# Performance work log

Measured on AMD Instinct MI355X. Metric: run time of the kernel, lower is better.

The kernel has to match this reference:

```python
import jax, jax.numpy as jnp
from jax import lax
import numpy as np

DN = ('NCHW', 'OIHW', 'NCHW')

def conv2d(x, w, b, stride=1, padding=1):
    out = lax.conv_general_dilated(
        x, w, window_strides=(stride, stride),
        padding=[(padding, padding), (padding, padding)],
        dimension_numbers=DN)
    return out + b[None, :, None, None]

def maxpool2d(x, k=2, s=2):
    return lax.reduce_window(x, -jnp.inf, lax.max,
                             window_dimensions=(1, 1, k, k),
                             window_strides=(1, 1, s, s),
                             padding='VALID')

def setup_inputs() -> dict:
    key = jax.random.key(0)
    ks = jax.random.split(key, 9)
    B = 4096
    x = jax.random.normal(ks[0], (B, 3, 32, 32), dtype=jnp.float32)
    # weights initialized like torch.randn(...) * 0.1, biases zeros
    w1 = jax.random.normal(ks[1], (16, 3, 3, 3), dtype=jnp.float32) * 0.1
    b1 = jnp.zeros((16,), jnp.float32)
    w2 = jax.random.normal(ks[2], (32, 16, 3, 3), dtype=jnp.float32) * 0.1
    b2 = jnp.zeros((32,), jnp.float32)
    w3 = jax.random.normal(ks[3], (64, 32, 3, 3), dtype=jnp.float32) * 0.1
    b3 = jnp.zeros((64,), jnp.float32)
    # fc: Linear(64*4*4, 10); kaiming-uniform-ish init
    fan_in = 64 * 4 * 4
    bound = 1.0 / np.sqrt(fan_in)
    fc_w = jax.random.uniform(ks[4], (10, fan_in), jnp.float32, -bound, bound)
    fc_b = jax.random.uniform(ks[5], (10,), jnp.float32, -bound, bound)
    return {"x": x, "w1": w1, "b1": b1, "w2": w2, "b2": b2,
            "w3": w3, "b3": b3, "fc_w": fc_w, "fc_b": fc_b}

def reference(x, w1, b1, w2, b2, w3, b3, fc_w, fc_b):
    h = maxpool2d(jax.nn.relu(conv2d(x, w1, b1)))   # [B,16,16,16]
    h = maxpool2d(jax.nn.relu(conv2d(h, w2, b2)))   # [B,32,8,8]
    h = maxpool2d(jax.nn.relu(conv2d(h, w3, b3)))   # [B,64,4,4]
    h = h.reshape(h.shape[0], -1)                    # [B,1024]
    # dropout is identity in eval mode
    return h @ fc_w.T + fc_b
```

## Files before the change

kernel.cpp:

```cpp
#include <hip/hip_runtime.h>

typedef float f32x4 __attribute__((ext_vector_type(4)));
typedef float f32x16v __attribute__((ext_vector_type(16)));
typedef __bf16 bf16x4 __attribute__((ext_vector_type(4)));
typedef __bf16 bf16x8 __attribute__((ext_vector_type(8)));

union U4B8 { uint4 u; bf16x8 b; };

#define B2P_OFF 0
#define B3P_OFF 9216
#define C1P_OFF 46080

__global__ __launch_bounds__(256) void pack_weights(
    const float* __restrict__ w1, const float* __restrict__ w2,
    const float* __restrict__ w3, __bf16* __restrict__ wsb) {
  int i = blockIdx.x * 256 + threadIdx.x;
  if (i < 9216) {
    int f = i >> 9, r = i & 511;
    int l = r >> 3, j = r & 7;
    int t = f >> 1, p = f & 1;
    int ky = t / 3, kx = t % 3;
    int oc = l & 31, ic = ((l >> 5) << 3) + j;
    float v = w2[oc * 144 + ic * 9 + ky * 3 + kx];
    __bf16 hi = (__bf16)v;
    wsb[B2P_OFF + i] = p ? (__bf16)(v - (float)hi) : hi;
  } else if (i < 9216 + 36864) {
    int q = i - 9216;
    int f = q >> 9, r = q & 511;
    int l = r >> 3, j = r & 7;
    int t = f >> 3, nt = (f >> 1) & 3, p = f & 1;
    int ky = t / 3, kx = t % 3;
    int oc = nt * 16 + (l & 15), ic = ((l >> 4) << 3) + j;
    float v = w3[oc * 288 + ic * 9 + ky * 3 + kx];
    __bf16 hi = (__bf16)v;
    wsb[B3P_OFF + q] = p ? (__bf16)(v - (float)hi) : hi;
  } else if (i < 9216 + 36864 + 1024) {
    int q = i - (9216 + 36864);
    int f = q >> 9, r = q & 511;
    int l = r >> 3, j = r & 7;
    int oc = l & 15, k = ((l >> 4) << 3) + j;
    float v = 0.f;
    if (k < 27) {
      int kx = k / 9, rem = k % 9;
      int ky = rem / 3, ic = rem % 3;
      v = w1[oc * 27 + ic * 9 + ky * 3 + kx];
    }
    __bf16 hi = (__bf16)v;
    wsb[C1P_OFF + q] = f ? (__bf16)(v - (float)hi) : hi;
  }
}

__global__ __launch_bounds__(256, 4) void cnn_fused(
    const float* __restrict__ x, const __bf16* __restrict__ wsb,
    const float* __restrict__ b1, const float* __restrict__ b2,
    const float* __restrict__ b3,
    const float* __restrict__ fcw, const float* __restrict__ fcb,
    float* __restrict__ out) {
  __shared__ __align__(16) unsigned char smem[16128];
  __bf16* s_img = (__bf16*)smem;
  __bf16* s2b   = (__bf16*)smem;
  __bf16* s3b   = (__bf16*)smem;
  float*  h3s   = (float*)(smem + 8960);

  const __bf16* b2p = wsb + B2P_OFF;
  const __bf16* b3p = wsb + B3P_OFF;
  const __bf16* c1p = wsb + C1P_OFF;

  const int tid = threadIdx.x;
  const int img = blockIdx.x;
  const int w = tid >> 6, lane = tid & 63;

  if (tid < 132) {
    int row, col;
    if (tid < 34)       { row = 0;        col = tid; }
    else if (tid < 68)  { row = 33;       col = tid - 34; }
    else if (tid < 100) { row = tid - 67; col = 0; }
    else                { row = tid - 99; col = 33; }
    *(unsigned long long*)&s_img[(row * 34 + col) * 4] = 0ull;
  }
  const float* xg = x + img * 3072;
  for (int i = tid; i < 1024; i += 256) {
    const int y = i >> 5, xx = i & 31;
    bf16x4 pk;
    pk.x = (__bf16)xg[i];
    pk.y = (__bf16)xg[i + 1024];
    pk.z = (__bf16)xg[i + 2048];
    pk.w = (__bf16)0.f;
    *(bf16x4*)&s_img[((y + 1) * 34 + (xx + 1)) * 4] = pk;
  }
  const bf16x8 B1h = *(const bf16x8*)(c1p + lane * 8);
  const bf16x8 B1l = *(const bf16x8*)(c1p + 512 + lane * 8);
  __syncthreads();

  float pooled[16];
  {
    const int xm = lane & 15, kg = lane >> 4;
    #pragma unroll
    for (int p = 0; p < 4; ++p) {
      f32x4 acc[2][2];
      #pragma unroll
      for (int ys = 0; ys < 2; ++ys)
        #pragma unroll
        for (int xh = 0; xh < 2; ++xh)
          #pragma unroll
          for (int r = 0; r < 4; ++r) acc[ys][xh][r] = 0.f;
      #pragma unroll
      for (int ys = 0; ys < 2; ++ys) {
        const int yqg = w * 8 + p * 2 + ys;
        #pragma unroll
        for (int xh = 0; xh < 2; ++xh) {
          const int xv = xh * 16 + xm;
          const int ca = xv + (kg <= 1 ? 0 : kg - 1);
          const int cb = xv + (kg < 2 ? 1 : 2);
          const uint2 qa0 = *(const uint2*)&s_img[((yqg + 0) * 34 + ca) * 4];
          const uint2 qa1 = *(const uint2*)&s_img[((yqg + 1) * 34 + ca) * 4];
          const uint2 qa2 = *(const uint2*)&s_img[((yqg + 2) * 34 + ca) * 4];
          const uint2 qb0 = *(const uint2*)&s_img[((yqg + 0) * 34 + cb) * 4];
          const uint2 qb1 = *(const uint2*)&s_img[((yqg + 1) * 34 + cb) * 4];
          const uint2 qb2 = *(const uint2*)&s_img[((yqg + 2) * 34 + cb) * 4];
          const uint a0 = qa0.x, a1 = qa0.y, a2 = qa1.x, a3 = qa1.y, a4 = qa2.x, a5 = qa2.y;
          const uint b0 = qb0.x, b1 = qb0.y, b2 = qb1.x, b3 = qb1.y, b4 = qb2.x;
          U4B8 A;
          A.u.x = kg == 0 ? a0
                : kg == 1 ? (a5 | (b0 << 16))
                : kg == 2 ? ((a4 >> 16) | (a5 << 16))
                :           a4;
          A.u.y = kg == 0 ? (a1 | (a2 << 16))
                : kg == 1 ? ((b0 >> 16) | (b1 << 16))
                : kg == 2 ? b0
                :           a5;
          A.u.z = kg == 0 ? ((a2 >> 16) | (a3 << 16))
                : kg == 1 ? b2
                : kg == 2 ? (b1 | (b2 << 16))
                :           0u;
          A.u.w = kg == 0 ? a4
                : kg == 1 ? (b3 | (b4 << 16))
                : kg == 2 ? ((b2 >> 16) | (b3 << 16))
                :           0u;
          acc[ys][xh] = __builtin_amdgcn_mfma_f32_16x16x32_bf16(A.b, B1h, acc[ys][xh], 0, 0, 0);
          acc[ys][xh] = __builtin_amdgcn_mfma_f32_16x16x32_bf16(A.b, B1l, acc[ys][xh], 0, 0, 0);
        }
      }
      #pragma unroll
      for (int xh = 0; xh < 2; ++xh)
        #pragma unroll
        for (int xp2 = 0; xp2 < 2; ++xp2) {
          const float v0 = fmaxf(acc[0][xh][xp2 * 2], acc[0][xh][xp2 * 2 + 1]);
          const float v1 = fmaxf(acc[1][xh][xp2 * 2], acc[1][xh][xp2 * 2 + 1]);
          pooled[p * 4 + xh * 2 + xp2] = fmaxf(v0, v1);
        }
    }
  }
  __syncthreads();

  if (tid < 68) {
    int row, col;
    if (tid < 18)      { row = 0;       col = tid; }
    else if (tid < 36) { row = 17;      col = tid - 18; }
    else if (tid < 52) { row = tid - 35; col = 0; }
    else               { row = tid - 51; col = 17; }
    unsigned long long* p = (unsigned long long*)&s2b[row * 448 + col * 24];
    p[0] = 0ull; p[1] = 0ull; p[2] = 0ull; p[3] = 0ull;
  }
  {
    const int oc = lane & 15, quad = lane >> 4;
    const float bias = b1[oc];
    #pragma unroll
    for (int p = 0; p < 4; ++p)
      #pragma unroll
      for (int xh = 0; xh < 2; ++xh)
        #pragma unroll
        for (int xp2 = 0; xp2 < 2; ++xp2) {
          const float v = fmaxf(pooled[p * 4 + xh * 2 + xp2] + bias, 0.f);
          const int py = w * 4 + p, px = xh * 8 + quad * 2 + xp2;
          s2b[(py + 1) * 448 + (px + 1) * 24 + oc] = (__bf16)v;
        }
  }
  bf16x8 Bf[18];
  #pragma unroll
  for (int f = 0; f < 18; ++f)
    Bf[f] = *(const bf16x8*)(b2p + f * 512 + lane * 8);
  __syncthreads();

  float pooled2[8];
  {
    const unsigned short* s2 = (const unsigned short*)s2b;
    const int xm = lane & 15, yoff = (lane >> 4) & 1, kh = lane >> 5;
    f32x16v acc0, acc1;
    #pragma unroll
    for (int r = 0; r < 16; ++r) { acc0[r] = 0.f; acc1[r] = 0.f; }
    #pragma unroll
    for (int t = 0; t < 9; ++t) {
      const int ky = t / 3, kx = t % 3;
      const int col = (xm + kx) * 24 + kh * 8;
      const int row0 = (4 * w + yoff + ky) * 448 + col;
      const int row1 = row0 + 896;
      bf16x8 a0h = *(const bf16x8*)&s2[row0];
      bf16x8 a1h = *(const bf16x8*)&s2[row1];
      acc0 = __builtin_amdgcn_mfma_f32_32x32x16_bf16(a0h, Bf[t * 2],     acc0, 0, 0, 0);
      acc1 = __builtin_amdgcn_mfma_f32_32x32x16_bf16(a1h, Bf[t * 2],     acc1, 0, 0, 0);
      acc0 = __builtin_amdgcn_mfma_f32_32x32x16_bf16(a0h, Bf[t * 2 + 1], acc0, 0, 0, 0);
      acc1 = __builtin_amdgcn_mfma_f32_32x32x16_bf16(a1h, Bf[t * 2 + 1], acc1, 0, 0, 0);
    }
    #pragma unroll
    for (int i2 = 0; i2 < 2; ++i2) {
      const f32x16v& a = i2 ? acc1 : acc0;
      #pragma unroll
      for (int bq = 0; bq < 2; ++bq)
        #pragma unroll
        for (int rq = 0; rq < 2; ++rq) {
          const int r0 = bq * 4 + rq * 2;
          pooled2[i2 * 4 + bq * 2 + rq] =
              fmaxf(fmaxf(a[r0], a[r0 + 1]), fmaxf(a[r0 + 8], a[r0 + 9]));
        }
    }
  }
  __syncthreads();

  if (tid < 36) {
    int row, col;
    if (tid < 10)      { row = 0;       col = tid; }
    else if (tid < 20) { row = 9;       col = tid - 10; }
    else if (tid < 28) { row = tid - 19; col = 0; }
    else               { row = tid - 27; col = 9; }
    unsigned long long* p = (unsigned long long*)&s3b[row * 448 + col * 40];
    #pragma unroll
    for (int u = 0; u < 8; ++u) p[u] = 0ull;
  }
  {
    const int oc = lane & 31, hh = lane >> 5;
    const float bias = b2[oc];
    #pragma unroll
    for (int i2 = 0; i2 < 2; ++i2)
      #pragma unroll
      for (int bq = 0; bq < 2; ++bq)
        #pragma unroll
        for (int rq = 0; rq < 2; ++rq) {
          const float v = fmaxf(pooled2[i2 * 4 + bq * 2 + rq] + bias, 0.f);
          const int py = 2 * w + i2, px = 2 * hh + 4 * bq + rq;
          s3b[(py + 1) * 448 + (px + 1) * 40 + oc] = (__bf16)v;
        }
  }
  __syncthreads();

  {
    const unsigned short* s3 = (const unsigned short*)s3b;
    const int nt = w;
    bf16x8 Bt[18];
    #pragma unroll
    for (int t = 0; t < 9; ++t) {
      Bt[t * 2]     = *(const bf16x8*)(b3p + (t * 8 + nt * 2) * 512 + lane * 8);
      Bt[t * 2 + 1] = *(const bf16x8*)(b3p + (t * 8 + nt * 2 + 1) * 512 + lane * 8);
    }
    const int m = lane & 15, quad = lane >> 4;
    const int xm = m & 7, yoff = m >> 3;
    f32x4 acc[4];
    #pragma unroll
    for (int mt = 0; mt < 4; ++mt)
      #pragma unroll
      for (int r = 0; r < 4; ++r) acc[mt][r] = 0.f;
    #pragma unroll
    for (int t = 0; t < 9; ++t) {
      const int ky = t / 3, kx = t % 3;
      #pragma unroll
      for (int mt = 0; mt < 4; ++mt) {
        const int ro = (2 * mt + yoff + ky) * 448 + (xm + kx) * 40 + quad * 8;
        bf16x8 ah = *(const bf16x8*)&s3[ro];
        acc[mt] = __builtin_amdgcn_mfma_f32_16x16x32_bf16(ah, Bt[t * 2],     acc[mt], 0, 0, 0);
        acc[mt] = __builtin_amdgcn_mfma_f32_16x16x32_bf16(ah, Bt[t * 2 + 1], acc[mt], 0, 0, 0);
      }
    }
    const int ocl = lane & 15;
    #pragma unroll
    for (int mt = 0; mt < 4; ++mt) {
      float p0 = fmaxf(acc[mt][0], acc[mt][1]);
      float p1 = fmaxf(acc[mt][2], acc[mt][3]);
      p0 = fmaxf(p0, __shfl_xor(p0, 32, 64));
      p1 = fmaxf(p1, __shfl_xor(p1, 32, 64));
      if (quad < 2) {
        const int oc = nt * 16 + ocl;
        const float bias = b3[oc];
        const int base = oc * 16 + mt * 4 + (quad & 1) * 2;
        h3s[base]     = fmaxf(p0 + bias, 0.f);
        h3s[base + 1] = fmaxf(p1 + bias, 0.f);
      }
    }
  }
  __syncthreads();

  if (w == 0) {
    float hv[16];
    #pragma unroll
    for (int i = 0; i < 16; ++i) hv[i] = h3s[i * 64 + lane];
    #pragma unroll
    for (int j = 0; j < 10; ++j) {
      float dot = 0.f;
      #pragma unroll
      for (int i = 0; i < 16; ++i)
        dot = fmaf(hv[i], fcw[j * 1024 + i * 64 + lane], dot);
      #pragma unroll
      for (int s = 32; s > 0; s >>= 1) dot += __shfl_xor(dot, s, 64);
      if (lane == 0) out[img * 10 + j] = dot + fcb[j];
    }
  }
}

extern "C" void kernel_launch(void* const* d_in, const int* in_sizes, int n_in,
                              void* d_out, int out_size, void* d_ws, size_t ws_size,
                              hipStream_t stream) {
  const float* x   = (const float*)d_in[0];
  const float* w1  = (const float*)d_in[1];
  const float* b1  = (const float*)d_in[2];
  const float* w2  = (const float*)d_in[3];
  const float* b2  = (const float*)d_in[4];
  const float* w3  = (const float*)d_in[5];
  const float* b3  = (const float*)d_in[6];
  const float* fcw = (const float*)d_in[7];
  const float* fcb = (const float*)d_in[8];
  __bf16* wsb = (__bf16*)d_ws;
  float* out = (float*)d_out;

  hipLaunchKernelGGL(pack_weights, dim3(184), dim3(256), 0, stream, w1, w2, w3, wsb);
  hipLaunchKernelGGL(cnn_fused, dim3(4096), dim3(256), 0, stream,
                     x, wsb, b1, b2, b3, fcw, fcb, out);
}
```

Baseline: 155.8 us.

## Process two images per block to amortize weight register loads

Each block now handles two images instead of one, halving the grid to 2048 blocks and doubling shared memory to about 32KB. The per-wave weight fragments for conv2 and conv3 are loaded into registers once and reused across both images, and the loop over images sits inside each stage, so barriers are shared as well. The FC stage uses two waves, one per image. The cost is more shared memory per block and more register pressure from the doubled pooled arrays, which could reduce occupancy, along with fewer blocks overall.

```diff
diff --git a/kernel.cpp b/kernel.cpp
--- a/kernel.cpp
+++ b/kernel.cpp
@@ -56,125 +56,134 @@
     const float* __restrict__ b3,
     const float* __restrict__ fcw, const float* __restrict__ fcb,
     float* __restrict__ out) {
-  __shared__ __align__(16) unsigned char smem[16128];
+  __shared__ __align__(16) unsigned char smem[32256];
   __bf16* s_img = (__bf16*)smem;
   __bf16* s2b   = (__bf16*)smem;
   __bf16* s3b   = (__bf16*)smem;
-  float*  h3s   = (float*)(smem + 8960);
+  float*  h3s   = (float*)(smem + 17920);
 
   const __bf16* b2p = wsb + B2P_OFF;
   const __bf16* b3p = wsb + B3P_OFF;
   const __bf16* c1p = wsb + C1P_OFF;
 
   const int tid = threadIdx.x;
-  const int img = blockIdx.x;
+  const int img0 = blockIdx.x * 2;
   const int w = tid >> 6, lane = tid & 63;
 
-  if (tid < 132) {
+  for (int i = tid; i < 264; i += 256) {
+    int ik = i >= 132, c = ik ? i - 132 : i;
     int row, col;
-    if (tid < 34)       { row = 0;        col = tid; }
-    else if (tid < 68)  { row = 33;       col = tid - 34; }
-    else if (tid < 100) { row = tid - 67; col = 0; }
-    else                { row = tid - 99; col = 33; }
-    *(unsigned long long*)&s_img[(row * 34 + col) * 4] = 0ull;
-  }
-  const float* xg = x + img * 3072;
-  for (int i = tid; i < 1024; i += 256) {
-    const int y = i >> 5, xx = i & 31;
+    if (c < 34)       { row = 0;       col = c; }
+    else if (c < 68)  { row = 33;      col = c - 34; }
+    else if (c < 100) { row = c - 67;  col = 0; }
+    else              { row = c - 99;  col = 33; }
+    *(unsigned long long*)&s_img[ik * 4624 + (row * 34 + col) * 4] = 0ull;
+  }
+  for (int i = tid; i < 2048; i += 256) {
+    const int ik = i >> 10, rem = i & 1023;
+    const int y = rem >> 5, xx = rem & 31;
+    const float* xg = x + (img0 + ik) * 3072;
     bf16x4 pk;
-    pk.x = (__bf16)xg[i];
-    pk.y = (__bf16)xg[i + 1024];
-    pk.z = (__bf16)xg[i + 2048];
+    pk.x = (__bf16)xg[rem];
+    pk.y = (__bf16)xg[rem + 1024];
+    pk.z = (__bf16)xg[rem + 2048];
     pk.w = (__bf16)0.f;
-    *(bf16x4*)&s_img[((y + 1) * 34 + (xx + 1)) * 4] = pk;
+    *(bf16x4*)&s_img[ik * 4624 + ((y + 1) * 34 + (xx + 1)) * 4] = pk;
   }
   const bf16x8 B1h = *(const bf16x8*)(c1p + lane * 8);
   const bf16x8 B1l = *(const bf16x8*)(c1p + 512 + lane * 8);
   __syncthreads();
 
-  float pooled[16];
+  float pooled[2][16];
   {
     const int xm = lane & 15, kg = lane >> 4;
     #pragma unroll
-    for (int p = 0; p < 4; ++p) {
-      f32x4 acc[2][2];
-      #pragma unroll
-      for (int ys = 0; ys < 2; ++ys)
+    for (int ik = 0; ik < 2; ++ik) {
+      const __bf16* si = s_img + ik * 4624;
+      #pragma unroll
+      for (int p = 0; p < 4; ++p) {
+        f32x4 acc[2][2];
+        #pragma unroll
+        for (int ys = 0; ys < 2; ++ys)
+          #pragma unroll
+          for (int xh = 0; xh < 2; ++xh)
+            #pragma unroll
+            for (int r = 0; r < 4; ++r) acc[ys][xh][r] = 0.f;
+        #pragma unroll
+        for (int ys = 0; ys < 2; ++ys) {
+          const int yqg = w * 8 + p * 2 + ys;
+          #pragma unroll
+          for (int xh = 0; xh < 2; ++xh) {
+            const int xv = xh * 16 + xm;
+            const int ca = xv + (kg <= 1 ? 0 : kg - 1);
+            const int cb = xv + (kg < 2 ? 1 : 2);
+            const uint2 qa0 = *(const uint2*)&si[((yqg + 0) * 34 + ca) * 4];
+            const uint2 qa1 = *(const uint2*)&si[((yqg + 1) * 34 + ca) * 4];
+            const uint2 qa2 = *(const uint2*)&si[((yqg + 2) * 34 + ca) * 4];
+            const uint2 qb0 = *(const uint2*)&si[((yqg + 0) * 34 + cb) * 4];
+            const uint2 qb1 = *(const uint2*)&si[((yqg + 1) * 34 + cb) * 4];
+            const uint2 qb2 = *(const uint2*)&si[((yqg + 2) * 34 + cb) * 4];
+            const uint a0 = qa0.x, a1 = qa0.y, a2 = qa1.x, a3 = qa1.y, a4 = qa2.x, a5 = qa2.y;
+            const uint b0 = qb0.x, b1 = qb0.y, b2 = qb1.x, b3 = qb1.y, b4 = qb2.x;
+            U4B8 A;
+            A.u.x = kg == 0 ? a0
+                  : kg == 1 ? (a5 | (b0 << 16))
+                  : kg == 2 ? ((a4 >> 16) | (a5 << 16))
+                  :           a4;
+            A.u.y = kg == 0 ? (a1 | (a2 << 16))
+                  : kg == 1 ? ((b0 >> 16) | (b1 << 16))
+                  : kg == 2 ? b0
+                  :           a5;
+            A.u.z = kg == 0 ? ((a2 >> 16) | (a3 << 16))
+                  : kg == 1 ? b2
+                  : kg == 2 ? (b1 | (b2 << 16))
+                  :           0u;
+            A.u.w = kg == 0 ? a4
+                  : kg == 1 ? (b3 | (b4 << 16))
+                  : kg == 2 ? ((b2 >> 16) | (b3 << 16))
+                  :           0u;
+            acc[ys][xh] = __builtin_amdgcn_mfma_f32_16x16x32_bf16(A.b, B1h, acc[ys][xh], 0, 0, 0);
+            acc[ys][xh] = __builtin_amdgcn_mfma_f32_16x16x32_bf16(A.b, B1l, acc[ys][xh], 0, 0, 0);
+          }
+        }
         #pragma unroll
         for (int xh = 0; xh < 2; ++xh)
           #pragma unroll
-          for (int r = 0; r < 4; ++r) acc[ys][xh][r] = 0.f;
-      #pragma unroll
-      for (int ys = 0; ys < 2; ++ys) {
-        const int yqg = w * 8 + p * 2 + ys;
-        #pragma unroll
-        for (int xh = 0; xh < 2; ++xh) {
-          const int xv = xh * 16 + xm;
-          const int ca = xv + (kg <= 1 ? 0 : kg - 1);
-          const int cb = xv + (kg < 2 ? 1 : 2);
-          const uint2 qa0 = *(const uint2*)&s_img[((yqg + 0) * 34 + ca) * 4];
-          const uint2 qa1 = *(const uint2*)&s_img[((yqg + 1) * 34 + ca) * 4];
-          const uint2 qa2 = *(const uint2*)&s_img[((yqg + 2) * 34 + ca) * 4];
-          const uint2 qb0 = *(const uint2*)&s_img[((yqg + 0) * 34 + cb) * 4];
-          const uint2 qb1 = *(const uint2*)&s_img[((yqg + 1) * 34 + cb) * 4];
-          const uint2 qb2 = *(const uint2*)&s_img[((yqg + 2) * 34 + cb) * 4];
-          const uint a0 = qa0.x, a1 = qa0.y, a2 = qa1.x, a3 = qa1.y, a4 = qa2.x, a5 = qa2.y;
-          const uint b0 = qb0.x, b1 = qb0.y, b2 = qb1.x, b3 = qb1.y, b4 = qb2.x;
-          U4B8 A;
-          A.u.x = kg == 0 ? a0
-                : kg == 1 ? (a5 | (b0 << 16))
-                : kg == 2 ? ((a4 >> 16) | (a5 << 16))
-                :           a4;
-          A.u.y = kg == 0 ? (a1 | (a2 << 16))
-                : kg == 1 ? ((b0 >> 16) | (b1 << 16))
-                : kg == 2 ? b0
-                :           a5;
-          A.u.z = kg == 0 ? ((a2 >> 16) | (a3 << 16))
-                : kg == 1 ? b2
-                : kg == 2 ? (b1 | (b2 << 16))
-                :           0u;
-          A.u.w = kg == 0 ? a4
-                : kg == 1 ? (b3 | (b4 << 16))
-                : kg == 2 ? ((b2 >> 16) | (b3 << 16))
-                :           0u;
-          acc[ys][xh] = __builtin_amdgcn_mfma_f32_16x16x32_bf16(A.b, B1h, acc[ys][xh], 0, 0, 0);
-          acc[ys][xh] = __builtin_amdgcn_mfma_f32_16x16x32_bf16(A.b, B1l, acc[ys][xh], 0, 0, 0);
-        }
-      }
-      #pragma unroll
-      for (int xh = 0; xh < 2; ++xh)
-        #pragma unroll
-        for (int xp2 = 0; xp2 < 2; ++xp2) {
-          const float v0 = fmaxf(acc[0][xh][xp2 * 2], acc[0][xh][xp2 * 2 + 1]);
-          const float v1 = fmaxf(acc[1][xh][xp2 * 2], acc[1][xh][xp2 * 2 + 1]);
-          pooled[p * 4 + xh * 2 + xp2] = fmaxf(v0, v1);
-        }
-    }
-  }
-  __syncthreads();
-
-  if (tid < 68) {
+          for (int xp2 = 0; xp2 < 2; ++xp2) {
+            const float v0 = fmaxf(acc[0][xh][xp2 * 2], acc[0][xh][xp2 * 2 + 1]);
+            const float v1 = fmaxf(acc[1][xh][xp2 * 2], acc[1][xh][xp2 * 2 + 1]);
+            pooled[ik][p * 4 + xh * 2 + xp2] = fmaxf(v0, v1);
+          }
+      }
+    }
+  }
+  __syncthreads();
+
+  if (tid < 136) {
+    int ik = tid >= 68, c = ik ? tid - 68 : tid;
     int row, col;
-    if (tid < 18)      { row = 0;       col = tid; }
-    else if (tid < 36) { row = 17;      col = tid - 18; }
-    else if (tid < 52) { row = tid - 35; col = 0; }
-    else               { row = tid - 51; col = 17; }
-    unsigned long long* p = (unsigned long long*)&s2b[row * 448 + col * 24];
+    if (c < 18)      { row = 0;       col = c; }
+    else if (c < 36) { row = 17;      col = c - 18; }
+    else if (c < 52) { row = c - 35;  col = 0; }
+    else             { row = c - 51;  col = 17; }
+    unsigned long long* p = (unsigned long long*)&s2b[ik * 8064 + row * 448 + col * 24];
     p[0] = 0ull; p[1] = 0ull; p[2] = 0ull; p[3] = 0ull;
   }
   {
     const int oc = lane & 15, quad = lane >> 4;
     const float bias = b1[oc];
     #pragma unroll
-    for (int p = 0; p < 4; ++p)
-      #pragma unroll
-      for (int xh = 0; xh < 2; ++xh)
-        #pragma unroll
-        for (int xp2 = 0; xp2 < 2; ++xp2) {
-          const float v = fmaxf(pooled[p * 4 + xh * 2 + xp2] + bias, 0.f);
-          const int py = w * 4 + p, px = xh * 8 + quad * 2 + xp2;
-          s2b[(py + 1) * 448 + (px + 1) * 24 + oc] = (__bf16)v;
-        }
+    for (int ik = 0; ik < 2; ++ik)
+      #pragma unroll
+      for (int p = 0; p < 4; ++p)
+        #pragma unroll
+        for (int xh = 0; xh < 2; ++xh)
+          #pragma unroll
+          for (int xp2 = 0; xp2 < 2; ++xp2) {
+            const float v = fmaxf(pooled[ik][p * 4 + xh * 2 + xp2] + bias, 0.f);
+            const int py = w * 4 + p, px = xh * 8 + quad * 2 + xp2;
+            s2b[ik * 8064 + (py + 1) * 448 + (px + 1) * 24 + oc] = (__bf16)v;
+          }
   }
   bf16x8 Bf[18];
   #pragma unroll
@@ -182,48 +191,52 @@
     Bf[f] = *(const bf16x8*)(b2p + f * 512 + lane * 8);
   __syncthreads();
 
-  float pooled2[8];
-  {
-    const unsigned short* s2 = (const unsigned short*)s2b;
+  float pooled2[2][8];
+  {
     const int xm = lane & 15, yoff = (lane >> 4) & 1, kh = lane >> 5;
-    f32x16v acc0, acc1;
-    #pragma unroll
-    for (int r = 0; r < 16; ++r) { acc0[r] = 0.f; acc1[r] = 0.f; }
-    #pragma unroll
-    for (int t = 0; t < 9; ++t) {
-      const int ky = t / 3, kx = t % 3;
-      const int col = (xm + kx) * 24 + kh * 8;
-      const int row0 = (4 * w + yoff + ky) * 448 + col;
-      const int row1 = row0 + 896;
-      bf16x8 a0h = *(const bf16x8*)&s2[row0];
-      bf16x8 a1h = *(const bf16x8*)&s2[row1];
-      acc0 = __builtin_amdgcn_mfma_f32_32x32x16_bf16(a0h, Bf[t * 2],     acc0, 0, 0, 0);
-      acc1 = __builtin_amdgcn_mfma_f32_32x32x16_bf16(a1h, Bf[t * 2],     acc1, 0, 0, 0);
-      acc0 = __builtin_amdgcn_mfma_f32_32x32x16_bf16(a0h, Bf[t * 2 + 1], acc0, 0, 0, 0);
-      acc1 = __builtin_amdgcn_mfma_f32_32x32x16_bf16(a1h, Bf[t * 2 + 1], acc1, 0, 0, 0);
-    }
-    #pragma unroll
-    for (int i2 = 0; i2 < 2; ++i2) {
-      const f32x16v& a = i2 ? acc1 : acc0;
-      #pragma unroll
-      for (int bq = 0; bq < 2; ++bq)
-        #pragma unroll
-        for (int rq = 0; rq < 2; ++rq) {
-          const int r0 = bq * 4 + rq * 2;
-          pooled2[i2 * 4 + bq * 2 + rq] =
-              fmaxf(fmaxf(a[r0], a[r0 + 1]), fmaxf(a[r0 + 8], a[r0 + 9]));
-        }
-    }
-  }
-  __syncthreads();
-
-  if (tid < 36) {
+    #pragma unroll
+    for (int ik = 0; ik < 2; ++ik) {
+      const unsigned short* s2 = (const unsigned short*)s2b + ik * 8064;
+      f32x16v acc0, acc1;
+      #pragma unroll
+      for (int r = 0; r < 16; ++r) { acc0[r] = 0.f; acc1[r] = 0.f; }
+      #pragma unroll
+      for (int t = 0; t < 9; ++t) {
+        const int ky = t / 3, kx = t % 3;
+        const int col = (xm + kx) * 24 + kh * 8;
+        const int row0 = (4 * w + yoff + ky) * 448 + col;
+        const int row1 = row0 + 896;
+        bf16x8 a0h = *(const bf16x8*)&s2[row0];
+        bf16x8 a1h = *(const bf16x8*)&s2[row1];
+        acc0 = __builtin_amdgcn_mfma_f32_32x32x16_bf16(a0h, Bf[t * 2],     acc0, 0, 0, 0);
+        acc1 = __builtin_amdgcn_mfma_f32_32x32x16_bf16(a1h, Bf[t * 2],     acc1, 0, 0, 0);
+        acc0 = __builtin_amdgcn_mfma_f32_32x32x16_bf16(a0h, Bf[t * 2 + 1], acc0, 0, 0, 0);
+        acc1 = __builtin_amdgcn_mfma_f32_32x32x16_bf16(a1h, Bf[t * 2 + 1], acc1, 0, 0, 0);
+      }
+      #pragma unroll
+      for (int i2 = 0; i2 < 2; ++i2) {
+        const f32x16v& a = i2 ? acc1 : acc0;
+        #pragma unroll
+        for (int bq = 0; bq < 2; ++bq)
+          #pragma unroll
+          for (int rq = 0; rq < 2; ++rq) {
+            const int r0 = bq * 4 + rq * 2;
+            pooled2[ik][i2 * 4 + bq * 2 + rq] =
+                fmaxf(fmaxf(a[r0], a[r0 + 1]), fmaxf(a[r0 + 8], a[r0 + 9]));
+          }
+      }
+    }
+  }
+  __syncthreads();
+
+  if (tid < 72) {
+    int ik = tid >= 36, c = ik ? tid - 36 : tid;
     int row, col;
-    if (tid < 10)      { row = 0;       col = tid; }
-    else if (tid < 20) { row = 9;       col = tid - 10; }
-    else if (tid < 28) { row = tid - 19; col = 0; }
-    else               { row = tid - 27; col = 9; }
-    unsigned long long* p = (unsigned long long*)&s3b[row * 448 + col * 40];
+    if (c < 10)      { row = 0;       col = c; }
+    else if (c < 20) { row = 9;       col = c - 10; }
+    else if (c < 28) { row = c - 19;  col = 0; }
+    else             { row = c - 27;  col = 9; }
+    unsigned long long* p = (unsigned long long*)&s3b[ik * 4480 + row * 448 + col * 40];
     #pragma unroll
     for (int u = 0; u < 8; ++u) p[u] = 0ull;
   }
@@ -231,20 +244,21 @@
     const int oc = lane & 31, hh = lane >> 5;
     const float bias = b2[oc];
     #pragma unroll
-    for (int i2 = 0; i2 < 2; ++i2)
-      #pragma unroll
-      for (int bq = 0; bq < 2; ++bq)
-        #pragma unroll
-        for (int rq = 0; rq < 2; ++rq) {
-          const float v = fmaxf(pooled2[i2 * 4 + bq * 2 + rq] + bias, 0.f);
-          const int py = 2 * w + i2, px = 2 * hh + 4 * bq + rq;
-          s3b[(py + 1) * 448 + (px + 1) * 40 + oc] = (__bf16)v;
-        }
-  }
-  __syncthreads();
-
-  {
-    const unsigned short* s3 = (const unsigned short*)s3b;
+    for (int ik = 0; ik < 2; ++ik)
+      #pragma unroll
+      for (int i2 = 0; i2 < 2; ++i2)
+        #pragma unroll
+        for (int bq = 0; bq < 2; ++bq)
+          #pragma unroll
+          for (int rq = 0; rq < 2; ++rq) {
+            const float v = fmaxf(pooled2[ik][i2 * 4 + bq * 2 + rq] + bias, 0.f);
+            const int py = 2 * w + i2, px = 2 * hh + 4 * bq + rq;
+            s3b[ik * 4480 + (py + 1) * 448 + (px + 1) * 40 + oc] = (__bf16)v;
+          }
+  }
+  __syncthreads();
+
+  {
     const int nt = w;
     bf16x8 Bt[18];
     #pragma unroll
@@ -254,44 +268,49 @@
     }
     const int m = lane & 15, quad = lane >> 4;
     const int xm = m & 7, yoff = m >> 3;
-    f32x4 acc[4];
-    #pragma unroll
-    for (int mt = 0; mt < 4; ++mt)
-      #pragma unroll
-      for (int r = 0; r < 4; ++r) acc[mt][r] = 0.f;
-    #pragma unroll
-    for (int t = 0; t < 9; ++t) {
-      const int ky = t / 3, kx = t % 3;
+    const int ocl = lane & 15;
+    #pragma unroll
+    for (int ik = 0; ik < 2; ++ik) {
+      const unsigned short* s3 = (const unsigned short*)s3b + ik * 4480;
+      f32x4 acc[4];
+      #pragma unroll
+      for (int mt = 0; mt < 4; ++mt)
+        #pragma unroll
+        for (int r = 0; r < 4; ++r) acc[mt][r] = 0.f;
+      #pragma unroll
+      for (int t = 0; t < 9; ++t) {
+        const int ky = t / 3, kx = t % 3;
+        #pragma unroll
+        for (int mt = 0; mt < 4; ++mt) {
+          const int ro = (2 * mt + yoff + ky) * 448 + (xm + kx) * 40 + quad * 8;
+          bf16x8 ah = *(const bf16x8*)&s3[ro];
+          acc[mt] = __builtin_amdgcn_mfma_f32_16x16x32_bf16(ah, Bt[t * 2],     acc[mt], 0, 0, 0);
+          acc[mt] = __builtin_amdgcn_mfma_f32_16x16x32_bf16(ah, Bt[t * 2 + 1], acc[mt], 0, 0, 0);
+        }
+      }
       #pragma unroll
       for (int mt = 0; mt < 4; ++mt) {
-        const int ro = (2 * mt + yoff + ky) * 448 + (xm + kx) * 40 + quad * 8;
-        bf16x8 ah = *(const bf16x8*)&s3[ro];
-        acc[mt] = __builtin_amdgcn_mfma_f32_16x16x32_bf16(ah, Bt[t * 2],     acc[mt], 0, 0, 0);
-        acc[mt] = __builtin_amdgcn_mfma_f32_16x16x32_bf16(ah, Bt[t * 2 + 1], acc[mt], 0, 0, 0);
-      }
-    }
-    const int ocl = lane & 15;
-    #pragma unroll
-    for (int mt = 0; mt < 4; ++mt) {
-      float p0 = fmaxf(acc[mt][0], acc[mt][1]);
-      float p1 = fmaxf(acc[mt][2], acc[mt][3]);
-      p0 = fmaxf(p0, __shfl_xor(p0, 32, 64));
-      p1 = fmaxf(p1, __shfl_xor(p1, 32, 64));
-      if (quad < 2) {
-        const int oc = nt * 16 + ocl;
-        const float bias = b3[oc];
-        const int base = oc * 16 + mt * 4 + (quad & 1) * 2;
-        h3s[base]     = fmaxf(p0 + bias, 0.f);
-        h3s[base + 1] = fmaxf(p1 + bias, 0.f);
-      }
-    }
-  }
-  __syncthreads();
-
-  if (w == 0) {
+        float p0 = fmaxf(acc[mt][0], acc[mt][1]);
+        float p1 = fmaxf(acc[mt][2], acc[mt][3]);
+        p0 = fmaxf(p0, __shfl_xor(p0, 32, 64));
+        p1 = fmaxf(p1, __shfl_xor(p1, 32, 64));
+        if (quad < 2) {
+          const int oc = nt * 16 + ocl;
+          const float bias = b3[oc];
+          const int base = ik * 1024 + oc * 16 + mt * 4 + (quad & 1) * 2;
+          h3s[base]     = fmaxf(p0 + bias, 0.f);
+          h3s[base + 1] = fmaxf(p1 + bias, 0.f);
+        }
+      }
+    }
+  }
+  __syncthreads();
+
+  if (w < 2) {
+    const float* h = h3s + w * 1024;
     float hv[16];
     #pragma unroll
-    for (int i = 0; i < 16; ++i) hv[i] = h3s[i * 64 + lane];
+    for (int i = 0; i < 16; ++i) hv[i] = h[i * 64 + lane];
     #pragma unroll
     for (int j = 0; j < 10; ++j) {
       float dot = 0.f;
@@ -300,7 +319,7 @@
         dot = fmaf(hv[i], fcw[j * 1024 + i * 64 + lane], dot);
       #pragma unroll
       for (int s = 32; s > 0; s >>= 1) dot += __shfl_xor(dot, s, 64);
-      if (lane == 0) out[img * 10 + j] = dot + fcb[j];
+      if (lane == 0) out[(img0 + w) * 10 + j] = dot + fcb[j];
     }
   }
 }
@@ -321,6 +340,6 @@
   float* out = (float*)d_out;
 
   hipLaunchKernelGGL(pack_weights, dim3(184), dim3(256), 0, stream, w1, w2, w3, wsb);
-  hipLaunchKernelGGL(cnn_fused, dim3(4096), dim3(256), 0, stream,
+  hipLaunchKernelGGL(cnn_fused, dim3(2048), dim3(256), 0, stream,
                      x, wsb, b1, b2, b3, fcw, fcb, out);
 }
```

Measured after the change: 178.1 us. +14.3%, slower.
